# Kernel optimization log

Measured on AMD Instinct MI355X. Metric: run time of the kernel, lower is better.

Reference implementation:

```python
import jax, jax.numpy as jnp
import numpy as np

FIR_KERNEL = (1, 3, 3, 1)
FACTOR = 2


def _setup_kernel(k):
    k = np.asarray(k, dtype=np.float32)
    if k.ndim == 1:
        k = np.outer(k, k)
    k /= np.sum(k)
    return k


def _fir_filter_2d(x, kf, pad0, pad1):
    # upfirdn2d with up=down=1: pad then depthwise-correlate with flipped FIR kernel.
    # x: [N, H, W, C], kf: [kh, kw]
    C = x.shape[3]
    x = jnp.pad(x, ((0, 0), (max(pad0, 0), max(pad1, 0)), (max(pad0, 0), max(pad1, 0)), (0, 0)))
    x = x[:, max(-pad0, 0): x.shape[1] - max(-pad1, 0), max(-pad0, 0): x.shape[2] - max(-pad1, 0), :]
    w = jnp.tile(jnp.asarray(kf[::-1, ::-1], x.dtype)[:, :, None, None], (1, 1, 1, C))
    return jax.lax.conv_general_dilated(
        x, w, window_strides=(1, 1), padding='VALID',
        dimension_numbers=('NHWC', 'HWIO', 'NHWC'), feature_group_count=C)


def _upsample_conv_2d(x, w, k, factor=2, gain=1.0):
    # StyleGAN2 fused upsample + conv: transposed 3x3 conv (stride=factor) then FIR filter.
    convH, convW, inC, outC = w.shape
    kf = _setup_kernel(k) * (gain * (factor ** 2))
    p = (kf.shape[0] - factor) - (convW - 1)
    num_groups = x.shape[3] // inC  # == 1 here
    # weight transform exactly as in up_or_down_sampling.upsample_conv_2d
    w = jnp.reshape(w, (convH, convW, inC, num_groups, -1))
    w = jnp.transpose(w[::-1, ::-1], (0, 1, 4, 3, 2))  # [cH, cW, outC, g, inC]
    w = jnp.reshape(w, (convH, convW, -1, num_groups * inC))
    x = jax.lax.conv_transpose(
        x, w, strides=(factor, factor), padding='VALID',
        transpose_kernel=True, dimension_numbers=('NHWC', 'HWIO', 'NHWC'))
    # [N, (H-1)*f+cH, (W-1)*f+cW, outC] -> FIR -> [N, 2H, 2W, outC]
    return _fir_filter_2d(x, kf, pad0=(p + 1) // 2 + factor - 1, pad1=p // 2 + 1)


def setup_inputs() -> dict:
    key = jax.random.key(0)
    k1, k2 = jax.random.split(key, 2)
    B, H, W, C = 4, 128, 128, 256
    out_ch = 256
    x = jax.random.normal(k1, (B, H, W, C), dtype=jnp.float32)
    # default_init(): variance_scaling(1., 'fan_avg', 'uniform')
    fan_avg = (3 * 3 * C + 3 * 3 * out_ch) / 2.0
    lim = float(np.sqrt(3.0 / fan_avg))
    w = jax.random.uniform(k2, (3, 3, C, out_ch), dtype=jnp.float32, minval=-lim, maxval=lim)
    b = jnp.zeros((out_ch,), dtype=jnp.float32)
    return {"x": x, "w": w, "b": b}


def reference(x, w, b):
    h = _upsample_conv_2d(x, w, FIR_KERNEL, factor=FACTOR)
    h = h + b.reshape(1, 1, 1, -1)
    return h
```

## Files before the change

kernel.cpp:

```cpp
#include <hip/hip_runtime.h>
#include <hip/hip_bf16.h>


typedef __attribute__((ext_vector_type(8))) __bf16 bf16x8;
typedef __attribute__((ext_vector_type(4))) float floatx4;

#define XP_ELEMS (4*130*130*256)
#define XP_BYTES (XP_ELEMS*2)
#define KT_ELEMS (1024*2304)

__device__ __forceinline__ void gl_lds16(const void* g, void* l) {
  __builtin_amdgcn_global_load_lds((const __attribute__((address_space(1))) void*)g,
                                   (__attribute__((address_space(3))) void*)l,
                                   16, 0, 0);
}

__global__ void pad_cast_kernel(const float* __restrict__ x,
                                __hip_bfloat16* __restrict__ xp) {
  int t = blockIdx.x * 256 + threadIdx.x;
  if (t >= 4*130*130*32) return;
  int c8  = (t & 31) << 3;
  int pix = t >> 5;
  int wc  = pix % 130;
  int tmp = pix / 130;
  int hr  = tmp % 130;
  int b   = tmp / 130;
  float vals[8] = {0.f,0.f,0.f,0.f,0.f,0.f,0.f,0.f};
  if (hr >= 1 && hr <= 128 && wc >= 1 && wc <= 128) {
    const float* s = x + (size_t)(((b*128 + (hr-1))*128 + (wc-1))*256 + c8);
    const float4 a = *(const float4*)s;
    const float4 c = *(const float4*)(s + 4);
    vals[0]=a.x; vals[1]=a.y; vals[2]=a.z; vals[3]=a.w;
    vals[4]=c.x; vals[5]=c.y; vals[6]=c.z; vals[7]=c.w;
  }
  __align__(16) __hip_bfloat16 o[8];
  #pragma unroll
  for (int i = 0; i < 8; ++i) o[i] = __float2bfloat16(vals[i]);
  *reinterpret_cast<uint4*>(xp + (size_t)t*8) = *reinterpret_cast<const uint4*>(o);
}

__global__ void make_kt_kernel(const float* __restrict__ w,
                               __hip_bfloat16* __restrict__ kt) {
  const int b     = blockIdx.x;
  const int ciblk = b & 7;
  const int tap   = (b >> 3) % 9;
  const int par   = b / 72;
  const int co    = threadIdx.x;
  const int pr = par >> 1, ps = par & 1;
  const int dy = tap / 3, dx = tap - dy*3;

  const float Atab[2][3][3] = {
    {{3.f,1.f,0.f},{1.f,3.f,3.f},{0.f,0.f,1.f}},
    {{1.f,0.f,0.f},{3.f,3.f,1.f},{0.f,1.f,3.f}}
  };

  float s[32];
  #pragma unroll
  for (int u = 0; u < 32; ++u) s[u] = 0.f;

  for (int i = 0; i < 3; ++i) {
    const float ay = Atab[pr][dy][i];
    if (ay == 0.f) continue;
    for (int j = 0; j < 3; ++j) {
      const float c = ay * Atab[ps][dx][j];
      if (c == 0.f) continue;
      const float* wp = w + ((size_t)(i*3 + j)*256 + ciblk*32)*256 + co;
      #pragma unroll
      for (int u = 0; u < 32; ++u)
        s[u] += c * wp[(size_t)u*256];
    }
  }

  __align__(16) __hip_bfloat16 o[32];
  #pragma unroll
  for (int u = 0; u < 32; ++u) o[u] = __float2bfloat16(s[u] * 0.0625f);
  __hip_bfloat16* dst = kt + (size_t)(par*256 + co)*2304 + tap*256 + ciblk*32;
  #pragma unroll
  for (int v = 0; v < 4; ++v)
    reinterpret_cast<uint4*>(dst)[v] = reinterpret_cast<const uint4*>(o)[v];
}

__global__ __launch_bounds__(256) void gemm_kernel(
    const __hip_bfloat16* __restrict__ xp,
    const __hip_bfloat16* __restrict__ kt,
    const float* __restrict__ bias,
    float* __restrict__ out)
{
  __shared__ __align__(16) __hip_bfloat16 sA[128*32];
  __shared__ __align__(16) __hip_bfloat16 sB[128*32];

  const int tid = threadIdx.x;
  const int bid = blockIdx.x;
  const int mt  = (bid & 7) + ((bid >> 6) << 3);
  const int nt  = (bid >> 3) & 7;
  const int b   = mt >> 7;
  const int ro  = mt & 127;
  const int n0  = nt << 7;

  const int wv   = tid >> 6;
  const int ln   = tid & 63;
  const int lm   = ln & 15;
  const int quad = ln >> 4;
  const int wm   = wv >> 1;
  const int wn   = wv & 1;

  const int sr    = tid >> 2;
  const int inner = (((tid & 3) ^ ((sr >> 1) & 3)) << 3);

  __hip_bfloat16* lA0 = sA + (wv*64)*8;
  __hip_bfloat16* lA1 = sA + (wv*64 + 256)*8;
  __hip_bfloat16* lB0 = sB + (wv*64)*8;
  __hip_bfloat16* lB1 = sB + (wv*64 + 256)*8;

  floatx4 acc[4][4];
  #pragma unroll
  for (int i = 0; i < 4; ++i)
    #pragma unroll
    for (int j = 0; j < 4; ++j)
      acc[i][j] = (floatx4){0.f, 0.f, 0.f, 0.f};

  const __hip_bfloat16* xb = xp + (size_t)(b*130)*130*256;
  const int cs = ((quad ^ ((lm >> 1) & 3)) << 3);

  for (int ks = 0; ks < 72; ++ks) {
    const int tap = ks >> 3;
    const int ci0 = (ks & 7) << 5;
    const int dy  = tap / 3;
    const int dx  = tap - dy*3;
    const int k0  = ks << 5;

    const __hip_bfloat16* gA = xb + (size_t)((ro + dy)*130 + dx + sr)*256 + ci0 + inner;
    gl_lds16(gA,            lA0);
    gl_lds16(gA + 64*256,   lA1);
    const __hip_bfloat16* gB = kt + (size_t)(n0 + sr)*2304 + k0 + inner;
    gl_lds16(gB,            lB0);
    gl_lds16(gB + 64*2304,  lB1);

    __syncthreads();

    bf16x8 af[4], bfr[4];
    #pragma unroll
    for (int i = 0; i < 4; ++i)
      af[i]  = *reinterpret_cast<const bf16x8*>(sA + (wm*64 + i*16 + lm)*32 + cs);
    #pragma unroll
    for (int i = 0; i < 4; ++i)
      bfr[i] = *reinterpret_cast<const bf16x8*>(sB + (wn*64 + i*16 + lm)*32 + cs);

    #pragma unroll
    for (int mi = 0; mi < 4; ++mi)
      #pragma unroll
      for (int ni = 0; ni < 4; ++ni)
        acc[mi][ni] = __builtin_amdgcn_mfma_f32_16x16x32_bf16(af[mi], bfr[ni], acc[mi][ni], 0, 0, 0);

    __syncthreads();
  }

  #pragma unroll
  for (int ni = 0; ni < 4; ++ni) {
    const int n   = n0 + wn*64 + ni*16 + lm;
    const int par = n >> 8;
    const int co  = n & 255;
    const int pr  = par >> 1;
    const int ps  = par & 1;
    const float bv = bias[co];
    const int rowo = b*256 + 2*ro + pr;
    #pragma unroll
    for (int mi = 0; mi < 4; ++mi) {
      const int so_b = wm*64 + mi*16 + (quad << 2);
      #pragma unroll
      for (int r = 0; r < 4; ++r) {
        const int so = so_b + r;
        out[((size_t)rowo*256 + (2*so + ps))*256 + co] = acc[mi][ni][r] + bv;
      }
    }
  }
}

extern "C" void kernel_launch(void* const* d_in, const int* in_sizes, int n_in,
                              void* d_out, int out_size, void* d_ws, size_t ws_size,
                              hipStream_t stream) {
  const float* x    = (const float*)d_in[0];
  const float* w    = (const float*)d_in[1];
  const float* bias = (const float*)d_in[2];
  float* out = (float*)d_out;

  __hip_bfloat16* xp = (__hip_bfloat16*)d_ws;
  __hip_bfloat16* kt = (__hip_bfloat16*)((char*)d_ws + XP_BYTES);

  pad_cast_kernel<<<(4*130*130*32 + 255)/256, 256, 0, stream>>>(x, xp);
  make_kt_kernel<<<288, 256, 0, stream>>>(w, kt);
  gemm_kernel<<<4096, 256, 0, stream>>>(xp, kt, bias, out);
}
```

Measured before the change: 638.5 us.

## Split upsample-conv into sub-pixel transposed-conv GEMM plus separate FIR pass

Replaces the fused 9-tap per-parity GEMM, where the FIR is folded into the weights, with two stages. The first stage is a transposed-conv GEMM that uses only the taps each sub-pixel parity needs (4/2/2/1 taps). It writes a bf16 intermediate of size 259x259 per image. A separate FIR kernel then applies the 4x4 separable filter and adds the bias. This cuts GEMM FLOPs roughly in half, at the cost of an extra intermediate round trip through memory (about 137MB written and read) and more kernel launches. It falls back to the old path when the workspace is too small.

```diff
diff --git a/kernel.cpp b/kernel.cpp
--- a/kernel.cpp
+++ b/kernel.cpp
@@ -6,7 +6,12 @@
 typedef __attribute__((ext_vector_type(4))) float floatx4;
 
 #define XP_ELEMS (4*130*130*256)
-#define XP_BYTES (XP_ELEMS*2)
+#define XP_BYTES ((size_t)XP_ELEMS*2)
+#define U_ELEMS  ((size_t)4*259*259*256)
+#define U_BYTES  (U_ELEMS*2)
+#define WQ_ELEMS 589824
+#define WQ_BYTES ((size_t)WQ_ELEMS*2)
+#define NEED_WS  (XP_BYTES + U_BYTES + WQ_BYTES)
 #define KT_ELEMS (1024*2304)
 
 __device__ __forceinline__ void gl_lds16(const void* g, void* l) {
@@ -39,25 +44,217 @@
   *reinterpret_cast<uint4*>(xp + (size_t)t*8) = *reinterpret_cast<const uint4*>(o);
 }
 
+__global__ void make_wq_kernel(const float* __restrict__ w,
+                               __hip_bfloat16* __restrict__ wq) {
+  int t = blockIdx.x * 256 + threadIdx.x;
+  int e, off, KE;
+  if (t < 262144)      { e=0; off=0;      KE=1024; }
+  else if (t < 393216) { e=1; off=262144; KE=512; }
+  else if (t < 524288) { e=2; off=393216; KE=512; }
+  else                 { e=3; off=524288; KE=256; }
+  int rel = t - off;
+  int co = rel / KE, k = rel - co*KE;
+  int tap = k >> 8, ci = k & 255;
+  const int iT[4][4] = {{2,2,0,0},{2,0,0,0},{1,1,0,0},{1,0,0,0}};
+  const int jT[4][4] = {{2,0,2,0},{1,1,0,0},{2,0,0,0},{1,0,0,0}};
+  int i = iT[e][tap], jx = jT[e][tap];
+  float v = w[((size_t)((i*3 + jx)*256 + ci))*256 + co] * 0.0625f;
+  wq[t] = __float2bfloat16(v);
+}
+
+__global__ void border_zero_kernel(__hip_bfloat16* __restrict__ U) {
+  const int bid = blockIdx.x;
+  const int b = bid / 517, p = bid % 517;
+  size_t idx;
+  if (p < 259) idx = (((size_t)b*259 + 0)*259 + p)*256;
+  else         idx = (((size_t)b*259 + (p - 259 + 1))*259 + 0)*256;
+  U[idx + threadIdx.x] = __float2bfloat16(0.f);
+}
+
+template<int E>
+__device__ __forceinline__ void stage1_body(const __hip_bfloat16* __restrict__ xp,
+                                            const __hip_bfloat16* __restrict__ wq,
+                                            __hip_bfloat16* __restrict__ U,
+                                            int mt, int nt,
+                                            __hip_bfloat16* sA, __hip_bfloat16* sB) {
+  constexpr int KE   = (E==0)?1024:(E==3)?256:512;
+  constexpr int NIT  = KE/32;
+  constexpr int WOFF = (E==0)?0:(E==1)?262144:(E==2)?393216:524288;
+  constexpr int EY = E>>1, EX = E&1;
+  constexpr int D1 = (E==1) ? -130 : -1;
+
+  const int tid = threadIdx.x;
+  const int b   = mt / 131;
+  const int mtb = mt - b*131;
+  const int n0  = nt << 7;
+
+  const int wv   = tid >> 6;
+  const int ln   = tid & 63;
+  const int lm   = ln & 15;
+  const int quad = ln >> 4;
+  const int wm   = wv >> 1;
+  const int wn   = wv & 1;
+
+  const int sr    = tid >> 2;
+  const int inner = (((tid & 3) ^ ((sr >> 1) & 3)) << 3);
+
+  const int mbase = mtb << 7;
+  int ms0 = mbase + sr;       if (ms0 > 16640) ms0 = 16640;
+  int ms1 = mbase + sr + 64;  if (ms1 > 16640) ms1 = 16640;
+  const int qy0 = ms0 / 129, qx0 = ms0 - qy0*129;
+  const int qy1 = ms1 / 129, qx1 = ms1 - qy1*129;
+  const int pix0 = (qy0 + 1)*130 + (qx0 + 1);
+  const int pix1 = (qy1 + 1)*130 + (qx1 + 1);
+
+  __hip_bfloat16* lA0 = sA + (wv*64)*8;
+  __hip_bfloat16* lA1 = sA + (wv*64 + 256)*8;
+  __hip_bfloat16* lB0 = sB + (wv*64)*8;
+  __hip_bfloat16* lB1 = sB + (wv*64 + 256)*8;
+
+  floatx4 acc[4][4];
+  #pragma unroll
+  for (int i = 0; i < 4; ++i)
+    #pragma unroll
+    for (int j = 0; j < 4; ++j)
+      acc[i][j] = (floatx4){0.f, 0.f, 0.f, 0.f};
+
+  const __hip_bfloat16* xb  = xp + (size_t)b*130*130*256;
+  const __hip_bfloat16* wqe = wq + WOFF;
+  const int cs = ((quad ^ ((lm >> 1) & 3)) << 3);
+
+  for (int ks = 0; ks < NIT; ++ks) {
+    const int tap = ks >> 3;
+    const int ci0 = (ks & 7) << 5;
+    const int k0  = ks << 5;
+    const int off = (tap == 0) ? 0 : (tap == 1) ? D1 : (tap == 2) ? -130 : -131;
+
+    gl_lds16(xb + (size_t)(pix0 + off)*256 + ci0 + inner, lA0);
+    gl_lds16(xb + (size_t)(pix1 + off)*256 + ci0 + inner, lA1);
+    gl_lds16(wqe + (size_t)(n0 + sr)*KE      + k0 + inner, lB0);
+    gl_lds16(wqe + (size_t)(n0 + sr + 64)*KE + k0 + inner, lB1);
+
+    __syncthreads();
+
+    bf16x8 af[4], bfr[4];
+    #pragma unroll
+    for (int i = 0; i < 4; ++i)
+      af[i]  = *reinterpret_cast<const bf16x8*>(sA + (wm*64 + i*16 + lm)*32 + cs);
+    #pragma unroll
+    for (int i = 0; i < 4; ++i)
+      bfr[i] = *reinterpret_cast<const bf16x8*>(sB + (wn*64 + i*16 + lm)*32 + cs);
+
+    #pragma unroll
+    for (int mi = 0; mi < 4; ++mi)
+      #pragma unroll
+      for (int ni = 0; ni < 4; ++ni)
+        acc[mi][ni] = __builtin_amdgcn_mfma_f32_16x16x32_bf16(af[mi], bfr[ni], acc[mi][ni], 0, 0, 0);
+
+    __syncthreads();
+  }
+
+  #pragma unroll
+  for (int ni = 0; ni < 4; ++ni) {
+    const int co = n0 + wn*64 + ni*16 + lm;
+    #pragma unroll
+    for (int mi = 0; mi < 4; ++mi) {
+      const int ml = wm*64 + mi*16 + (quad << 2);
+      #pragma unroll
+      for (int r = 0; r < 4; ++r) {
+        const int m = mbase + ml + r;
+        if (m <= 16640) {
+          const int qy = m / 129, qx = m - qy*129;
+          const int R = 2*qy + EY + 1, C = 2*qx + EX + 1;
+          U[(((size_t)b*259 + R)*259 + C)*256 + co] = __float2bfloat16(acc[mi][ni][r]);
+        }
+      }
+    }
+  }
+}
+
+__global__ __launch_bounds__(256) void stage1_kernel(const __hip_bfloat16* __restrict__ xp,
+                                                     const __hip_bfloat16* __restrict__ wq,
+                                                     __hip_bfloat16* __restrict__ U) {
+  __shared__ __align__(16) __hip_bfloat16 sA[128*32];
+  __shared__ __align__(16) __hip_bfloat16 sB[128*32];
+  const int bid = blockIdx.x;
+  const int mt = (bid & 7) + ((bid >> 6) << 3);
+  if (mt >= 524) return;
+  const int g = (bid >> 3) & 7;
+  const int e = g >> 1, nt = g & 1;
+  switch (e) {
+    case 0: stage1_body<0>(xp, wq, U, mt, nt, sA, sB); break;
+    case 1: stage1_body<1>(xp, wq, U, mt, nt, sA, sB); break;
+    case 2: stage1_body<2>(xp, wq, U, mt, nt, sA, sB); break;
+    default: stage1_body<3>(xp, wq, U, mt, nt, sA, sB); break;
+  }
+}
+
+__global__ __launch_bounds__(256) void fir_kernel(const __hip_bfloat16* __restrict__ U,
+                                                  const float* __restrict__ bias,
+                                                  float* __restrict__ out) {
+  const int bid = blockIdx.x, tid = threadIdx.x;
+  const int b = bid >> 11, i = (bid >> 4) & 127, jb = bid & 15;
+  const int c8 = tid & 31, jj = tid >> 5;
+  const int j = jb*8 + jj, co = c8 << 3;
+  const __hip_bfloat16* Ub = U + (((size_t)b*259 + 2*i)*259 + 2*j)*256 + co;
+
+  float ve[5][8], vo[5][8];
+  #pragma unroll
+  for (int dx = 0; dx < 5; ++dx) {
+    float r[5][8];
+    #pragma unroll
+    for (int dy = 0; dy < 5; ++dy) {
+      uint4 q = *reinterpret_cast<const uint4*>(Ub + ((size_t)(dy*259 + dx) << 8));
+      const unsigned* w32 = reinterpret_cast<const unsigned*>(&q);
+      #pragma unroll
+      for (int t = 0; t < 4; ++t) {
+        r[dy][2*t]   = __uint_as_float(w32[t] << 16);
+        r[dy][2*t+1] = __uint_as_float(w32[t] & 0xffff0000u);
+      }
+    }
+    #pragma unroll
+    for (int k = 0; k < 8; ++k) {
+      ve[dx][k] = (r[0][k] + r[3][k]) + 3.f*(r[1][k] + r[2][k]);
+      vo[dx][k] = (r[1][k] + r[4][k]) + 3.f*(r[2][k] + r[3][k]);
+    }
+  }
+  float bv[8];
+  *(float4*)bv     = *(const float4*)(bias + co);
+  *(float4*)(bv+4) = *(const float4*)(bias + co + 4);
+  float o[4][8];
+  #pragma unroll
+  for (int k = 0; k < 8; ++k) {
+    o[0][k] = (ve[0][k]+ve[3][k]) + 3.f*(ve[1][k]+ve[2][k]) + bv[k];
+    o[1][k] = (ve[1][k]+ve[4][k]) + 3.f*(ve[2][k]+ve[3][k]) + bv[k];
+    o[2][k] = (vo[0][k]+vo[3][k]) + 3.f*(vo[1][k]+vo[2][k]) + bv[k];
+    o[3][k] = (vo[1][k]+vo[4][k]) + 3.f*(vo[2][k]+vo[3][k]) + bv[k];
+  }
+  #pragma unroll
+  for (int pr = 0; pr < 2; ++pr)
+    #pragma unroll
+    for (int ps = 0; ps < 2; ++ps) {
+      float* op = out + (((size_t)(b*256 + 2*i + pr))*256 + (2*j + ps))*256 + co;
+      *(float4*)op     = *(float4*)&o[pr*2+ps][0];
+      *(float4*)(op+4) = *(float4*)&o[pr*2+ps][4];
+    }
+}
+
 __global__ void make_kt_kernel(const float* __restrict__ w,
                                __hip_bfloat16* __restrict__ kt) {
-  const int b     = blockIdx.x;
-  const int ciblk = b & 7;
-  const int tap   = (b >> 3) % 9;
-  const int par   = b / 72;
+  const int bb    = blockIdx.x;
+  const int ciblk = bb & 7;
+  const int tap   = (bb >> 3) % 9;
+  const int par   = bb / 72;
   const int co    = threadIdx.x;
   const int pr = par >> 1, ps = par & 1;
   const int dy = tap / 3, dx = tap - dy*3;
-
   const float Atab[2][3][3] = {
     {{3.f,1.f,0.f},{1.f,3.f,3.f},{0.f,0.f,1.f}},
     {{1.f,0.f,0.f},{3.f,3.f,1.f},{0.f,1.f,3.f}}
   };
-
   float s[32];
   #pragma unroll
   for (int u = 0; u < 32; ++u) s[u] = 0.f;
-
   for (int i = 0; i < 3; ++i) {
     const float ay = Atab[pr][dy][i];
     if (ay == 0.f) continue;
@@ -66,11 +263,9 @@
       if (c == 0.f) continue;
       const float* wp = w + ((size_t)(i*3 + j)*256 + ciblk*32)*256 + co;
       #pragma unroll
-      for (int u = 0; u < 32; ++u)
-        s[u] += c * wp[(size_t)u*256];
-    }
-  }
-
+      for (int u = 0; u < 32; ++u) s[u] += c * wp[(size_t)u*256];
+    }
+  }
   __align__(16) __hip_bfloat16 o[32];
   #pragma unroll
   for (int u = 0; u < 32; ++u) o[u] = __float2bfloat16(s[u] * 0.0625f);
@@ -84,11 +279,9 @@
     const __hip_bfloat16* __restrict__ xp,
     const __hip_bfloat16* __restrict__ kt,
     const float* __restrict__ bias,
-    float* __restrict__ out)
-{
+    float* __restrict__ out) {
   __shared__ __align__(16) __hip_bfloat16 sA[128*32];
   __shared__ __align__(16) __hip_bfloat16 sB[128*32];
-
   const int tid = threadIdx.x;
   const int bid = blockIdx.x;
   const int mt  = (bid & 7) + ((bid >> 6) << 3);
@@ -96,48 +289,35 @@
   const int b   = mt >> 7;
   const int ro  = mt & 127;
   const int n0  = nt << 7;
-
-  const int wv   = tid >> 6;
-  const int ln   = tid & 63;
-  const int lm   = ln & 15;
-  const int quad = ln >> 4;
-  const int wm   = wv >> 1;
-  const int wn   = wv & 1;
-
-  const int sr    = tid >> 2;
+  const int wv = tid >> 6, ln = tid & 63, lm = ln & 15, quad = ln >> 4;
+  const int wm = wv >> 1, wn = wv & 1;
+  const int sr = tid >> 2;
   const int inner = (((tid & 3) ^ ((sr >> 1) & 3)) << 3);
-
   __hip_bfloat16* lA0 = sA + (wv*64)*8;
   __hip_bfloat16* lA1 = sA + (wv*64 + 256)*8;
   __hip_bfloat16* lB0 = sB + (wv*64)*8;
   __hip_bfloat16* lB1 = sB + (wv*64 + 256)*8;
-
   floatx4 acc[4][4];
   #pragma unroll
   for (int i = 0; i < 4; ++i)
     #pragma unroll
     for (int j = 0; j < 4; ++j)
       acc[i][j] = (floatx4){0.f, 0.f, 0.f, 0.f};
-
   const __hip_bfloat16* xb = xp + (size_t)(b*130)*130*256;
   const int cs = ((quad ^ ((lm >> 1) & 3)) << 3);
-
   for (int ks = 0; ks < 72; ++ks) {
     const int tap = ks >> 3;
     const int ci0 = (ks & 7) << 5;
     const int dy  = tap / 3;
     const int dx  = tap - dy*3;
     const int k0  = ks << 5;
-
     const __hip_bfloat16* gA = xb + (size_t)((ro + dy)*130 + dx + sr)*256 + ci0 + inner;
     gl_lds16(gA,            lA0);
     gl_lds16(gA + 64*256,   lA1);
     const __hip_bfloat16* gB = kt + (size_t)(n0 + sr)*2304 + k0 + inner;
     gl_lds16(gB,            lB0);
     gl_lds16(gB + 64*2304,  lB1);
-
     __syncthreads();
-
     bf16x8 af[4], bfr[4];
     #pragma unroll
     for (int i = 0; i < 4; ++i)
@@ -145,16 +325,13 @@
     #pragma unroll
     for (int i = 0; i < 4; ++i)
       bfr[i] = *reinterpret_cast<const bf16x8*>(sB + (wn*64 + i*16 + lm)*32 + cs);
-
     #pragma unroll
     for (int mi = 0; mi < 4; ++mi)
       #pragma unroll
       for (int ni = 0; ni < 4; ++ni)
         acc[mi][ni] = __builtin_amdgcn_mfma_f32_16x16x32_bf16(af[mi], bfr[ni], acc[mi][ni], 0, 0, 0);
-
     __syncthreads();
   }
-
   #pragma unroll
   for (int ni = 0; ni < 4; ++ni) {
     const int n   = n0 + wn*64 + ni*16 + lm;
@@ -185,9 +362,19 @@
   float* out = (float*)d_out;
 
   __hip_bfloat16* xp = (__hip_bfloat16*)d_ws;
-  __hip_bfloat16* kt = (__hip_bfloat16*)((char*)d_ws + XP_BYTES);
-
-  pad_cast_kernel<<<(4*130*130*32 + 255)/256, 256, 0, stream>>>(x, xp);
-  make_kt_kernel<<<288, 256, 0, stream>>>(w, kt);
-  gemm_kernel<<<4096, 256, 0, stream>>>(xp, kt, bias, out);
-}
+
+  if (ws_size >= NEED_WS) {
+    __hip_bfloat16* U  = (__hip_bfloat16*)((char*)d_ws + XP_BYTES);
+    __hip_bfloat16* wq = (__hip_bfloat16*)((char*)d_ws + XP_BYTES + U_BYTES);
+    pad_cast_kernel<<<8450, 256, 0, stream>>>(x, xp);
+    make_wq_kernel<<<2304, 256, 0, stream>>>(w, wq);
+    border_zero_kernel<<<2068, 256, 0, stream>>>(U);
+    stage1_kernel<<<4224, 256, 0, stream>>>(xp, wq, U);
+    fir_kernel<<<8192, 256, 0, stream>>>(U, bias, out);
+  } else {
+    __hip_bfloat16* kt = (__hip_bfloat16*)((char*)d_ws + XP_BYTES);
+    pad_cast_kernel<<<8450, 256, 0, stream>>>(x, xp);
+    make_kt_kernel<<<288, 256, 0, stream>>>(w, kt);
+    gemm_kernel<<<4096, 256, 0, stream>>>(xp, kt, bias, out);
+  }
+}
```

New measurement: 585.6 us. 8.3% less time.
